# Kernel optimization log

Measured on AMD Instinct MI355X. Metric: run time of the kernel, lower is better.

The kernel has to match this reference:

```python
import math
import jax, jax.numpy as jnp
import numpy as np

NHEAD = 4
EPS = 1e-5


def make_pe(max_len, d):
    pos = np.arange(max_len, dtype=np.float32)[:, None]
    div = np.exp(np.arange(0, d, 2, dtype=np.float32) * (-math.log(10000.0) / d))
    pe = np.zeros((max_len, d), np.float32)
    pe[:, 0::2] = np.sin(pos * div)
    pe[:, 1::2] = np.cos(pos * div)
    return jnp.asarray(pe)


def layer_norm(x, g, b):
    m = jnp.mean(x, axis=-1, keepdims=True)
    v = jnp.mean((x - m) ** 2, axis=-1, keepdims=True)
    return (x - m) / jnp.sqrt(v + EPS) * g + b


def mha(q, k, v, wq, bq, wk, bk, wv, bv, wo, bo, kmask=None):
    # q: [b, Lq, d], k/v: [b, Lk, d]
    b_, lq, d = q.shape
    lk = k.shape[1]
    hd = d // NHEAD
    qh = (q @ wq + bq).reshape(b_, lq, NHEAD, hd)
    kh = (k @ wk + bk).reshape(b_, lk, NHEAD, hd)
    vh = (v @ wv + bv).reshape(b_, lk, NHEAD, hd)
    s = jnp.einsum('bqhd,bkhd->bhqk', qh, kh) / jnp.sqrt(jnp.float32(hd))
    if kmask is not None:
        s = jnp.where(kmask[None, None, None, :], s, jnp.float32(-1e9))
    a = jax.nn.softmax(s, axis=-1)
    o = jnp.einsum('bhqk,bkhd->bqhd', a, vh).reshape(b_, lq, d)
    return o @ wo + bo


def _forward(src, in_w, in_b, dec_start,
             e_wq, e_bq, e_wk, e_bk, e_wv, e_bv, e_wo, e_bo,
             e_ln1_g, e_ln1_b, e_w1, e_b1, e_w2, e_b2, e_ln2_g, e_ln2_b,
             d_swq, d_sbq, d_swk, d_sbk, d_swv, d_sbv, d_swo, d_sbo,
             d_ln1_g, d_ln1_b,
             d_cwq, d_cbq, d_cwk, d_cbk, d_cwv, d_cbv, d_cwo, d_cbo,
             d_ln2_g, d_ln2_b,
             d_w1, d_b1, d_w2, d_b2, d_ln3_g, d_ln3_b,
             out_w, out_b, tgt_len):
    B, S = src.shape
    d = in_w.shape[1]
    T = tgt_len
    pe = make_pe(max(S, T) + 10, d)

    # ---- encoder (1 post-norm layer, relu FFN, dropout off) ----
    x = (src[..., None] @ in_w + in_b) * jnp.sqrt(jnp.float32(d))  # [B,S,d]
    x = x + pe[None, :S]
    x = layer_norm(x + mha(x, x, x, e_wq, e_bq, e_wk, e_bk, e_wv, e_bv, e_wo, e_bo), e_ln1_g, e_ln1_b)
    mem = layer_norm(x + (jax.nn.relu(x @ e_w1 + e_b1) @ e_w2 + e_b2), e_ln2_g, e_ln2_b)

    buf0 = jnp.zeros((B, T + 1, d), src.dtype).at[:, 0].set(dec_start[0, 0])
    pe_dec = pe[None, :T + 1]
    kidx = jnp.arange(T + 1)

    def step(buf, t):
        di = buf + pe_dec
        kmask = kidx <= t  # full (non-causal) attention over the t+1 valid tokens
        h = layer_norm(di + mha(di, di, di, d_swq, d_sbq, d_swk, d_sbk,
                                d_swv, d_sbv, d_swo, d_sbo, kmask=kmask),
                       d_ln1_g, d_ln1_b)
        h = layer_norm(h + mha(h, mem, mem, d_cwq, d_cbq, d_cwk, d_cbk,
                               d_cwv, d_cbv, d_cwo, d_cbo),
                       d_ln2_g, d_ln2_b)
        h = layer_norm(h + (jax.nn.relu(h @ d_w1 + d_b1) @ d_w2 + d_b2),
                       d_ln3_g, d_ln3_b)
        last = h[:, t]                       # [B,d] output at the newest position
        buf = buf.at[:, t + 1].set(last)     # feed back as next decoder token
        y = (last @ out_w + out_b)[:, 0]     # [B]
        return buf, y

    _, outs = jax.lax.scan(step, buf0, jnp.arange(T))  # outs: [T,B]
    return outs.T  # [B,T]


def setup_inputs():
    B, S, T, d, ff = 128, 512, 64, 48, 128
    ks = iter(jax.random.split(jax.random.key(0), 64))

    def w(shape, s=0.08):
        return jax.random.normal(next(ks), shape, jnp.float32) * s

    ones = lambda: jnp.ones((d,), jnp.float32)
    zeros = lambda: jnp.zeros((d,), jnp.float32)
    return dict(
        src=jax.random.normal(next(ks), (B, S), jnp.float32),
        in_w=w((1, d)), in_b=w((d,)),
        dec_start=w((1, 1, d), 1.0),
        e_wq=w((d, d)), e_bq=w((d,)), e_wk=w((d, d)), e_bk=w((d,)),
        e_wv=w((d, d)), e_bv=w((d,)), e_wo=w((d, d)), e_bo=w((d,)),
        e_ln1_g=ones(), e_ln1_b=zeros(),
        e_w1=w((d, ff)), e_b1=w((ff,)), e_w2=w((ff, d)), e_b2=w((d,)),
        e_ln2_g=ones(), e_ln2_b=zeros(),
        d_swq=w((d, d)), d_sbq=w((d,)), d_swk=w((d, d)), d_sbk=w((d,)),
        d_swv=w((d, d)), d_sbv=w((d,)), d_swo=w((d, d)), d_sbo=w((d,)),
        d_ln1_g=ones(), d_ln1_b=zeros(),
        d_cwq=w((d, d)), d_cbq=w((d,)), d_cwk=w((d, d)), d_cbk=w((d,)),
        d_cwv=w((d, d)), d_cbv=w((d,)), d_cwo=w((d, d)), d_cbo=w((d,)),
        d_ln2_g=ones(), d_ln2_b=zeros(),
        d_w1=w((d, ff)), d_b1=w((ff,)), d_w2=w((ff, d)), d_b2=w((d,)),
        d_ln3_g=ones(), d_ln3_b=zeros(),
        out_w=w((d, 1)), out_b=w((1,)),
        tgt_len=T,
    )


def reference(src, in_w, in_b, dec_start,
              e_wq, e_bq, e_wk, e_bk, e_wv, e_bv, e_wo, e_bo,
              e_ln1_g, e_ln1_b, e_w1, e_b1, e_w2, e_b2, e_ln2_g, e_ln2_b,
              d_swq, d_sbq, d_swk, d_sbk, d_swv, d_sbv, d_swo, d_sbo,
              d_ln1_g, d_ln1_b,
              d_cwq, d_cbq, d_cwk, d_cbk, d_cwv, d_cbv, d_cwo, d_cbo,
              d_ln2_g, d_ln2_b,
              d_w1, d_b1, d_w2, d_b2, d_ln3_g, d_ln3_b,
              out_w, out_b, tgt_len):
    return _forward(src, in_w, in_b, dec_start,
                    e_wq, e_bq, e_wk, e_bk, e_wv, e_bv, e_wo, e_bo,
                    e_ln1_g, e_ln1_b, e_w1, e_b1, e_w2, e_b2, e_ln2_g, e_ln2_b,
                    d_swq, d_sbq, d_swk, d_sbk, d_swv, d_sbv, d_swo, d_sbo,
                    d_ln1_g, d_ln1_b,
                    d_cwq, d_cbq, d_cwk, d_cbk, d_cwv, d_cbv, d_cwo, d_cbo,
                    d_ln2_g, d_ln2_b,
                    d_w1, d_b1, d_w2, d_b2, d_ln3_g, d_ln3_b,
                    out_w, out_b, tgt_len)
```

## Files before the change

kernel.cpp:

```cpp
#include <hip/hip_runtime.h>
#include <hip/hip_bf16.h>
#include <hip/hip_fp16.h>


constexpr int kB  = 128;
constexpr int kS  = 512;
constexpr int kT  = 64;
constexpr int kD  = 48;
constexpr int kFF = 128;
constexpr int kNH = 4;
constexpr int kHD = 12;

__device__ __forceinline__ void wsync(){
  __builtin_amdgcn_wave_barrier();
  asm volatile("" ::: "memory");
}

template<int CTRL,int RM,int BM,bool BC>
__device__ __forceinline__ float dppmov(float x, float old){
  return __builtin_bit_cast(float, __builtin_amdgcn_update_dpp(
      __builtin_bit_cast(int, old), __builtin_bit_cast(int, x), CTRL, RM, BM, BC));
}
__device__ __forceinline__ float wsum(float x){
  x += dppmov<0x111,0xf,0xf,true>(x, 0.f);
  x += dppmov<0x112,0xf,0xf,true>(x, 0.f);
  x += dppmov<0x114,0xf,0xf,true>(x, 0.f);
  x += dppmov<0x118,0xf,0xf,true>(x, 0.f);
  x += dppmov<0x142,0xa,0xf,true>(x, 0.f);
  x += dppmov<0x143,0xc,0xf,true>(x, 0.f);
  return __builtin_bit_cast(float, __builtin_amdgcn_readlane(__builtin_bit_cast(int, x), 63));
}
__device__ __forceinline__ float rowsum16(float x){
  x += dppmov<0x111,0xf,0xf,true>(x, 0.f);
  x += dppmov<0x112,0xf,0xf,true>(x, 0.f);
  x += dppmov<0x114,0xf,0xf,true>(x, 0.f);
  x += dppmov<0x118,0xf,0xf,true>(x, 0.f);
  return x;
}

__device__ __forceinline__ float pe_val(int p, int j){
  int i = j >> 1;
  float f = expf(-0.19188209108283716f * (float)(2*i));
  float a = (float)p * f;
  return (j & 1) ? cosf(a) : sinf(a);
}
__device__ __forceinline__ float pe_fast(int p, int j){
  int i = j >> 1;
  float f = __expf(-0.19188209108283716f * (float)(2*i));
  float a = (float)p * f;
  return (j & 1) ? __cosf(a) : __sinf(a);
}

typedef _Float16 h2v __attribute__((ext_vector_type(2)));
union H2U { __half2 h; h2v v; };
__device__ __forceinline__ float fdot2(__half2 a, __half2 b, float c){
#if __has_builtin(__builtin_amdgcn_fdot2)
  H2U ua, ub; ua.h=a; ub.h=b;
  return __builtin_amdgcn_fdot2(ua.v, ub.v, c, false);
#else
  float2 fa=__half22float2(a), fb=__half22float2(b);
  return fmaf(fa.y, fb.y, fmaf(fa.x, fb.x, c));
#endif
}

__device__ __forceinline__ float dot48d(const __half2* x, const __half* w){
  const __half2* w2=(const __half2*)w;
  float a0=0.f,a1=0.f,a2=0.f,a3=0.f;
  #pragma unroll
  for(int c=0;c<6;c++){
    a0=fdot2(x[4*c+0],w2[4*c+0],a0);
    a1=fdot2(x[4*c+1],w2[4*c+1],a1);
    a2=fdot2(x[4*c+2],w2[4*c+2],a2);
    a3=fdot2(x[4*c+3],w2[4*c+3],a3);
  }
  return (a0+a1)+(a2+a3);
}
__device__ __forceinline__ float dot128d(const __half2* x, const __half* w){
  const __half2* w2=(const __half2*)w;
  float a0=0.f,a1=0.f,a2=0.f,a3=0.f,a4=0.f,a5=0.f,a6=0.f,a7=0.f;
  #pragma unroll
  for(int c=0;c<8;c++){
    a0=fdot2(x[8*c+0],w2[8*c+0],a0);
    a1=fdot2(x[8*c+1],w2[8*c+1],a1);
    a2=fdot2(x[8*c+2],w2[8*c+2],a2);
    a3=fdot2(x[8*c+3],w2[8*c+3],a3);
    a4=fdot2(x[8*c+4],w2[8*c+4],a4);
    a5=fdot2(x[8*c+5],w2[8*c+5],a5);
    a6=fdot2(x[8*c+6],w2[8*c+6],a6);
    a7=fdot2(x[8*c+7],w2[8*c+7],a7);
  }
  return ((a0+a1)+(a2+a3))+((a4+a5)+(a6+a7));
}

__global__ void __launch_bounds__(256) k_qkv(const float* __restrict__ src,
    const float* __restrict__ in_w, const float* __restrict__ in_b,
    float* __restrict__ X0,
    const float* __restrict__ wq, const float* __restrict__ bq,
    const float* __restrict__ wk, const float* __restrict__ bk,
    const float* __restrict__ wv, const float* __restrict__ bv,
    __half* __restrict__ Q, __half* __restrict__ K, __half* __restrict__ V){
  __shared__ __align__(16) __half W[3*2688];
  __shared__ __align__(16) float bias[3*kD];
  __shared__ __align__(16) __half2 xt2[32*24];
  int tid = threadIdx.x;
  for (int i=tid;i<3*2304;i+=256){ int m=i/2304, e=i%2304, k=e/48, j=e%48;
    const float* w = (m==0)?wq:((m==1)?wk:wv);
    W[m*2688 + j*56 + k] = __float2half(w[e]); }
  for (int i=tid;i<3*kD;i+=256){ int m=i/kD,e=i%kD;
    const float* w=(m==0)?bq:((m==1)?bk:bv); bias[i]=w[e]; }
  long row0 = (long)blockIdx.x*32;
  const float sc = 6.928203230275509f;
  for (int i=tid;i<768;i+=256){
    int r=i/24, c=i%24;
    long gr=row0+r; int s=(int)(gr&511);
    float sv=src[gr];
    float va=(sv*in_w[2*c  ]+in_b[2*c  ])*sc + pe_fast(s,2*c  );
    float vb=(sv*in_w[2*c+1]+in_b[2*c+1])*sc + pe_fast(s,2*c+1);
    ((float2*)X0)[row0*24 + i]=make_float2(va,vb);
    xt2[i]=__floats2half2_rn(va,vb);
  }
  __syncthreads();
  int r = tid>>3, c0 = tid&7;
  __half2 xr[24];
  #pragma unroll
  for(int u=0;u<24;u++) xr[u]=xt2[r*24+u];
  for (int c=c0; c<3*kD; c+=8){
    int m=c/kD, j=c%kD;
    float acc = bias[m*kD+j] + dot48d(xr, W + m*2688 + j*56);
    __half* o = (m==0)?Q:((m==1)?K:V);
    o[(row0+r)*kD+j]=__float2half(acc);
  }
}

__global__ void __launch_bounds__(256) k_attn(const __half* Q, const __half* __restrict__ K,
                       const __half* __restrict__ V, __half* O){
  int b = blockIdx.x / kNH, h = blockIdx.x % kNH;
  __shared__ __align__(16) __half2 Ks2[kS*6];
  __shared__ __align__(16) float   Vs[kS*kHD];
  int tid = threadIdx.x;
  long base = ((long)b*kS)*kD + h*kHD;
  for (int i=tid;i<kS*6;i+=256){ int r=i/6, c=i%6;
    Ks2[i]=*(const __half2*)&K[base+(long)r*kD+2*c]; }
  for (int i=tid;i<kS*kHD;i+=256){ int r=i/kHD, d=i%kHD;
    Vs[i]=__half2float(V[base+(long)r*kD+d]); }
  const float rs = 0.28867513459481287f;
  int q0 = tid, q1 = tid+256;
  __half2 qa2[6], qb2[6];
  {
    const __half2* qp0=(const __half2*)(Q+base+(long)q0*kD);
    const __half2* qp1=(const __half2*)(Q+base+(long)q1*kD);
    #pragma unroll
    for(int c=0;c<6;c++){ qa2[c]=qp0[c]; qb2[c]=qp1[c]; }
  }
  __syncthreads();
  float2 acc0[6], acc1[6];
  #pragma unroll
  for(int j=0;j<6;j++){ acc0[j]=make_float2(0.f,0.f); acc1[j]=make_float2(0.f,0.f); }
  float l0=0.f, l1=0.f;
  for(int k=0;k<kS;k++){
    const __half2* kp=Ks2+k*6;
    float sA0=0.f,sA1=0.f,sB0=0.f,sB1=0.f;
    #pragma unroll
    for(int c=0;c<3;c++){
      sA0=fdot2(qa2[2*c],kp[2*c],sA0); sA1=fdot2(qa2[2*c+1],kp[2*c+1],sA1);
      sB0=fdot2(qb2[2*c],kp[2*c],sB0); sB1=fdot2(qb2[2*c+1],kp[2*c+1],sB1);
    }
    float p0=__expf((sA0+sA1)*rs), p1=__expf((sB0+sB1)*rs);
    l0+=p0; l1+=p1;
    const float2* vp=(const float2*)(Vs+k*kHD);
    #pragma unroll
    for(int j=0;j<6;j++){
      float2 v=vp[j];
      acc0[j].x=fmaf(p0,v.x,acc0[j].x); acc0[j].y=fmaf(p0,v.y,acc0[j].y);
      acc1[j].x=fmaf(p1,v.x,acc1[j].x); acc1[j].y=fmaf(p1,v.y,acc1[j].y);
    }
  }
  float i0=1.f/l0, i1=1.f/l1;
  #pragma unroll
  for(int j=0;j<6;j++){
    O[base+(long)q0*kD+2*j  ]=__float2half(acc0[j].x*i0);
    O[base+(long)q0*kD+2*j+1]=__float2half(acc0[j].y*i0);
    O[base+(long)q1*kD+2*j  ]=__float2half(acc1[j].x*i1);
    O[base+(long)q1*kD+2*j+1]=__float2half(acc1[j].y*i1);
  }
}

__global__ void __launch_bounds__(256) k_oproj_ln(const float* __restrict__ Xres, const __half* __restrict__ O,
      const float* __restrict__ wo, const float* __restrict__ bo,
      const float* __restrict__ g, const float* __restrict__ bb,
      __half* __restrict__ Xout){
  __shared__ __align__(16) __half W[kD*56];
  __shared__ float bsh[kD], gs[kD], bs2[kD];
  __shared__ __align__(16) float res[32*kD];
  __shared__ __align__(16) __half2 ot2[32*24];
  __shared__ float mrow[32], rstd[32];
  int tid=threadIdx.x;
  for(int i=tid;i<kD*kD;i+=256){ int k=i/48, j=i%48; W[j*56+k]=__float2half(wo[i]); }
  if(tid<kD){ bsh[tid]=bo[tid]; gs[tid]=g[tid]; bs2[tid]=bb[tid]; }
  long row0=(long)blockIdx.x*32;
  const __half2* Op=(const __half2*)(O+row0*kD);
  for(int i=tid;i<768;i+=256) ot2[i]=Op[i];
  __syncthreads();
  int r=tid>>3, c0=tid&7;
  __half2 orow[24];
  #pragma unroll
  for(int u=0;u<24;u++) orow[u]=ot2[r*24+u];
  for(int j=c0;j<kD;j+=8){
    float acc=bsh[j]+dot48d(orow, W+j*56);
    res[r*kD+j]=Xres[row0*kD + r*kD + j]+acc;
  }
  __syncthreads();
  if(tid<32){
    float s=0.f, s2=0.f;
    for(int j=0;j<kD;j++){ float v=res[tid*kD+j]; s+=v; s2+=v*v; }
    float m=s*(1.f/kD);
    mrow[tid]=m; rstd[tid]=rsqrtf(s2*(1.f/kD)-m*m+1e-5f);
  }
  __syncthreads();
  for(int i=tid;i<32*kD;i+=256){int r2=i/kD,j=i%kD;
    Xout[row0*kD+i]=__float2half((res[i]-mrow[r2])*rstd[r2]*gs[j]+bs2[j]); }
}

__global__ void __launch_bounds__(256) k_ffn_ln(const __half* __restrict__ Xin,
   const float* __restrict__ w1, const float* __restrict__ b1,
   const float* __restrict__ w2, const float* __restrict__ b2,
   const float* __restrict__ g, const float* __restrict__ bb,
   float* __restrict__ Xout){
  __shared__ __align__(16) __half W1[kFF*56];
  __shared__ __align__(16) __half W2[kD*136];
  __shared__ float b1s[kFF], b2s[kD], gs[kD], bs2[kD];
  __shared__ __align__(16) __half xt[16*kD];
  __shared__ __align__(16) __half h1h[16*kFF];
  __shared__ __align__(16) float res[16*kD];
  __shared__ float mrow[16], rstd[16];
  int tid=threadIdx.x;
  for(int i=tid;i<kD*kFF;i+=256){ int k=i/128, c=i%128; W1[c*56+k]=__float2half(w1[i]); }
  for(int i=tid;i<kFF*kD;i+=256){ int u=i/48, j=i%48; W2[j*136+u]=__float2half(w2[i]); }
  if(tid<kFF) b1s[tid]=b1[tid];
  if(tid<kD){ b2s[tid]=b2[tid]; gs[tid]=g[tid]; bs2[tid]=bb[tid]; }
  long row0=(long)blockIdx.x*16;
  const __half2* Xp=(const __half2*)(Xin+row0*kD);
  for(int i=tid;i<384;i+=256) ((__half2*)xt)[i]=Xp[i];
  __syncthreads();
  int r=tid>>4, c0=tid&15;
  {
    __half2 xr[24];
    const __half2* xp=(const __half2*)(xt + r*kD);
    #pragma unroll
    for(int u=0;u<24;u++) xr[u]=xp[u];
    for(int c=c0;c<kFF;c+=16){
      float acc=b1s[c]+dot48d(xr, W1+c*56);
      h1h[r*kFF+c]=__float2half(fmaxf(acc,0.f));
    }
  }
  __syncthreads();
  {
    const __half2* hp=(const __half2*)(h1h + r*kFF);
    for(int j=c0;j<kD;j+=16){
      float acc=b2s[j]+dot128d(hp, W2+j*136);
      res[r*kD+j]=__half2float(xt[r*kD+j])+acc;
    }
  }
  __syncthreads();
  if(tid<16){
    float s=0.f, s2=0.f;
    for(int j=0;j<kD;j++){ float v=res[tid*kD+j]; s+=v; s2+=v*v; }
    float m=s*(1.f/kD);
    mrow[tid]=m; rstd[tid]=rsqrtf(s2*(1.f/kD)-m*m+1e-5f);
  }
  __syncthreads();
  for(int i=tid;i<16*kD;i+=256){int r2=i/kD,j=i%kD;
    Xout[row0*kD+i]=(res[i]-mrow[r2])*rstd[r2]*gs[j]+bs2[j]; }
}

__global__ void __launch_bounds__(256) k_ckv(const float* __restrict__ M,
    const float* __restrict__ wk, const float* __restrict__ bk,
    const float* __restrict__ wv, const float* __restrict__ bv,
    __half* __restrict__ Kc, __half* __restrict__ Vc){
  __shared__ __align__(16) __half W[2*2688];
  __shared__ float bias[2*kD];
  __shared__ __align__(16) __half2 xt2[32*24];
  int tid=threadIdx.x;
  for(int i=tid;i<2*2304;i+=256){ int m=i/2304, e=i%2304, k=e/48, j=e%48;
    W[m*2688 + j*56 + k] = __float2half((m?wv:wk)[e]); }
  for(int i=tid;i<2*kD;i+=256){ int m=i/kD,e=i%kD; bias[i]=(m?bv:bk)[e]; }
  long row0=(long)blockIdx.x*32;
  const float2* Mp=(const float2*)(M+row0*kD);
  for(int i=tid;i<768;i+=256){ float2 v=Mp[i]; xt2[i]=__floats2half2_rn(v.x,v.y); }
  __syncthreads();
  int r=tid>>3, c0=tid&7;
  __half2 xr[24];
  #pragma unroll
  for(int u=0;u<24;u++) xr[u]=xt2[r*24+u];
  long gr=row0+r; long bb2=gr>>9; long s=gr&511;
  for(int c=c0;c<2*kD;c+=8){
    int m=c/kD, j=c%kD;
    float acc=bias[m*kD+j]+dot48d(xr, W+m*2688+j*56);
    if(m==0) Kc[(bb2*kS+s)*kD + j]=__float2half(acc);
    else     Vc[(bb2*kD+j)*kS + s]=__float2half(acc);
  }
}

__global__ void k_prep(const float* __restrict__ swq,const float* __restrict__ swk,
                       const float* __restrict__ swv,const float* __restrict__ swo,
                       const float* __restrict__ cwq,const float* __restrict__ cwo,
                       const float* __restrict__ w1,const float* __restrict__ w2,
                       __half* __restrict__ Wh){
  int idx=blockIdx.x*256+threadIdx.x;
  if(idx>=26112) return;
  if(idx<13824){
    int m=idx/2304, e=idx%2304, j=e/48, k=e%48;
    const float* w = (m==0)?swq:((m==1)?swk:((m==2)?swv:((m==3)?swo:((m==4)?cwq:cwo))));
    Wh[m*2688 + j*56 + k] = __float2half(w[k*48+j]);
  } else if(idx<19968){
    int e=idx-13824, c=e/48, k=e%48;
    Wh[16128 + c*56 + k] = __float2half(w1[k*128+c]);
  } else {
    int e=idx-19968, j=e/128, u=e%128;
    Wh[23296 + j*136 + u] = __float2half(w2[u*48+j]);
  }
}

struct DecP {
  const float *dec_start, *sbq, *sbk, *sbv, *sbo, *ln1g, *ln1b,
              *cbq, *cbo, *ln2g, *ln2b, *fb1, *fb2, *ln3g, *ln3b, *ow, *ob;
};

__global__ void __launch_bounds__(256,1) k_dec(const __half* __restrict__ KT,
    const __half* __restrict__ VT, const __half* __restrict__ Wg, DecP P,
    float* __restrict__ out){
  __shared__ __align__(16) __half Wl[29824];
  __shared__ __align__(16) float peT[kT*kD];
  __shared__ __align__(16) __half KhH[kNH*kT*kHD];
  __shared__ __align__(16) float  Vh[kNH*kT*kHD];
  __shared__ __align__(16) __half qSH[kNH*kHD];
  __shared__ __align__(16) __half xvH[kD], soH[kD], h1H[kD], cqH[kD], covH[kD], h2H[kD];
  __shared__ __align__(16) __half f1H[kFF];
  int tid=threadIdx.x, b=blockIdx.x, wave=tid>>6, lane=tid&63;
  const float rs=0.28867513459481287f;

  for(int i=tid;i<29824/8;i+=256) ((float4*)Wl)[i]=((const float4*)Wg)[i];
  for(int i=tid;i<kT*kD;i+=256){ int tt=i/kD, j=i%kD; peT[i]=pe_val(tt,j); }

  float c_sbq=0,c_sbk=0,c_sbv=0, c_bo=0,c_cbq=0,c_cbo=0,c_fb2=0;
  float g1=0,bb1=0,g2=0,bb2=0,g3=0,bb3=0,c_ow=0, c_fb1a=0,c_fb1b=0, c_ds=0;
  if(wave==0){
    if(lane<kD){
      c_ds=P.dec_start[lane];
      c_sbq=P.sbq[lane]; c_sbk=P.sbk[lane]; c_sbv=P.sbv[lane];
      c_bo=P.sbo[lane]; c_cbq=P.cbq[lane]; c_cbo=P.cbo[lane]; c_fb2=P.fb2[lane];
      g1=P.ln1g[lane]; bb1=P.ln1b[lane];
      g2=P.ln2g[lane]; bb2=P.ln2b[lane];
      g3=P.ln3g[lane]; bb3=P.ln3b[lane];
      c_ow=P.ow[lane];
    }
    c_fb1a=P.fb1[lane]; c_fb1b=P.fb1[lane+64];
  }
  float c_ob=P.ob[0];

  __half2 Kr2[4][2][6], Vr2[4][kHD];
  {
    const __half* Kb = KT + (long)b*kS*kD;
    const __half2* Vb = (const __half2*)VT + (long)b*kD*(kS/2);
    #pragma unroll
    for(int i=0;i<4;i++){
      int sp = lane + 64*i;
      #pragma unroll
      for(int e=0;e<2;e++){
        const __half2* kp=(const __half2*)(Kb + (long)(2*sp+e)*kD + wave*kHD);
        #pragma unroll
        for(int c=0;c<6;c++) Kr2[i][e][c]=kp[c];
      }
      #pragma unroll
      for(int u=0;u<kHD;u++) Vr2[i][u]=Vb[(wave*kHD+u)*(kS/2)+sp];
    }
  }
  __syncthreads();

  float xv=0;
  if(wave==0 && lane<kD){ xv=c_ds+peT[lane]; xvH[lane]=__float2half(xv); }
  __syncthreads();

  float h1=0, h2=0, yacc=0;
  for(int t=0;t<kT;t++){
    if(wave==0){
      if(lane<kD){
        __half2 xr[24];
        const __half2* xp=(const __half2*)xvH;
        #pragma unroll
        for(int u=0;u<24;u++) xr[u]=xp[u];
        float qv=c_sbq+dot48d(xr, Wl + 0*2688 + lane*56);
        float kv=c_sbk+dot48d(xr, Wl + 1*2688 + lane*56);
        float vv=c_sbv+dot48d(xr, Wl + 2*2688 + lane*56);
        int hh=lane/kHD, dd=lane%kHD;
        qSH[lane]=__float2half(qv);
        KhH[(hh*kT+t)*kHD+dd]=__float2half(kv);
        Vh[(hh*kT+t)*kHD+dd]=vv;
      }
      wsync();
      {
        int hh=lane>>4, g=lane&15;
        __half2 q2[6];
        const __half2* qp=(const __half2*)qSH + hh*6;
        #pragma unroll
        for(int c=0;c<6;c++) q2[c]=qp[c];
        float l=0.f, acc[kHD];
        #pragma unroll
        for(int u=0;u<kHD;u++) acc[u]=0.f;
        #pragma unroll
        for(int kk=0;kk<4;kk++){
          int key=g+16*kk;
          if(key<=t){
            const __half2* kp=(const __half2*)KhH + (hh*kT+key)*6;
            float a0=0.f,a1=0.f;
            a0=fdot2(q2[0],kp[0],a0); a1=fdot2(q2[1],kp[1],a1);
            a0=fdot2(q2[2],kp[2],a0); a1=fdot2(q2[3],kp[3],a1);
            a0=fdot2(q2[4],kp[4],a0); a1=fdot2(q2[5],kp[5],a1);
            float p=__expf((a0+a1)*rs);
            l+=p;
            const float4* vp=(const float4*)(Vh+(hh*kT+key)*kHD);
            float4 v0=vp[0], v1=vp[1], v2=vp[2];
            float vr[kHD]={v0.x,v0.y,v0.z,v0.w,v1.x,v1.y,v1.z,v1.w,v2.x,v2.y,v2.z,v2.w};
            #pragma unroll
            for(int u=0;u<kHD;u++) acc[u]+=p*vr[u];
          }
        }
        l=rowsum16(l);
        #pragma unroll
        for(int u=0;u<kHD;u++) acc[u]=rowsum16(acc[u]);
        if(g==15){
          float inv=1.f/l;
          #pragma unroll
          for(int u=0;u<6;u++)
            ((__half2*)soH)[hh*6+u]=__floats2half2_rn(acc[2*u]*inv, acc[2*u+1]*inv);
        }
      }
      wsync();
      {
        float rr=0.f;
        if(lane<kD)
          rr=xv+c_bo+dot48d((const __half2*)soH, Wl+8064+lane*56);
        float s1=wsum(rr), s2=wsum(rr*rr);
        float mean=s1*(1.f/48.f);
        float rstd=rsqrtf(s2*(1.f/48.f)-mean*mean+1e-5f);
        h1=0;
        if(lane<kD){ h1=(rr-mean)*rstd*g1+bb1; h1H[lane]=__float2half(h1); }
      }
      wsync();
      if(lane<kD)
        cqH[lane]=__float2half(c_cbq+dot48d((const __half2*)h1H, Wl+10752+lane*56));
    }
    __syncthreads();
    {
      __half2 q2[6];
      #pragma unroll
      for(int c=0;c<6;c++) q2[c]=((const __half2*)cqH)[wave*6+c];
      float s[8];
      #pragma unroll
      for(int i=0;i<4;i++){
        #pragma unroll
        for(int e=0;e<2;e++){
          float a0=0.f,a1=0.f;
          const __half2* kp=Kr2[i][e];
          a0=fdot2(q2[0],kp[0],a0); a1=fdot2(q2[1],kp[1],a1);
          a0=fdot2(q2[2],kp[2],a0); a1=fdot2(q2[3],kp[3],a1);
          a0=fdot2(q2[4],kp[4],a0); a1=fdot2(q2[5],kp[5],a1);
          s[2*i+e]=(a0+a1)*rs;
        }
      }
      float p32[8], l=0.f;
      #pragma unroll
      for(int j=0;j<8;j++){ p32[j]=__expf(s[j]); l+=p32[j]; }
      l=wsum(l);
      float inv=1.f/l;
      __half2 ph[4];
      #pragma unroll
      for(int i=0;i<4;i++) ph[i]=__floats2half2_rn(p32[2*i]*inv, p32[2*i+1]*inv);
      float acc[kHD];
      #pragma unroll
      for(int u=0;u<kHD;u++) acc[u]=0.f;
      #pragma unroll
      for(int i=0;i<4;i++){
        #pragma unroll
        for(int u=0;u<kHD;u++) acc[u]=fdot2(ph[i],Vr2[i][u],acc[u]);
      }
      #pragma unroll
      for(int u=0;u<kHD;u++) acc[u]=wsum(acc[u]);
      if(lane==0){
        #pragma unroll
        for(int u=0;u<6;u++)
          ((__half2*)covH)[wave*6+u]=__floats2half2_rn(acc[2*u], acc[2*u+1]);
      }
    }
    __syncthreads();
    if(wave==0){
      {
        float rr=0.f;
        if(lane<kD)
          rr=h1+c_cbo+dot48d((const __half2*)covH, Wl+13440+lane*56);
        float s1=wsum(rr), s2=wsum(rr*rr);
        float mean=s1*(1.f/48.f);
        float rstd=rsqrtf(s2*(1.f/48.f)-mean*mean+1e-5f);
        h2=0;
        if(lane<kD){ h2=(rr-mean)*rstd*g2+bb2; h2H[lane]=__float2half(h2); }
      }
      wsync();
      {
        float a=c_fb1a+dot48d((const __half2*)h2H, Wl+16128+lane*56);
        float bcol=c_fb1b+dot48d((const __half2*)h2H, Wl+16128+(lane+64)*56);
        f1H[lane]=__float2half(fmaxf(a,0.f));
        f1H[lane+64]=__float2half(fmaxf(bcol,0.f));
      }
      wsync();
      {
        float rr=0.f;
        if(lane<kD)
          rr=h2+c_fb2+dot128d((const __half2*)f1H, Wl+23296+lane*136);
        float s1=wsum(rr), s2=wsum(rr*rr);
        float mean=s1*(1.f/48.f);
        float rstd=rsqrtf(s2*(1.f/48.f)-mean*mean+1e-5f);
        float cv=0.f;
        if(lane<kD) cv=(rr-mean)*rstd*g3+bb3;
        if(lane<kD && t+1<kT){ xv=cv+peT[(t+1)*kD+lane]; xvH[lane]=__float2half(xv); }
        wsync();
        float y=wsum(cv*c_ow);
        if(lane==t) yacc=y;
      }
    }
  }
  if(wave==0) out[(long)b*kT+lane]=yacc+c_ob;
}

extern "C" void kernel_launch(void* const* d_in, const int* in_sizes, int n_in,
                              void* d_out, int out_size, void* d_ws, size_t ws_size,
                              hipStream_t stream){
  float* ws = (float*)d_ws;
  __half* Wh = (__half*)ws;
  const size_t NB = (size_t)kB*kS*kD;
  float*  A  = ws + 16384;
  __half* H1 = (__half*)(A + NB);
  __half* H2 = H1 + NB;
  __half* H3 = H2 + NB;

  k_qkv  <<<(kB*kS)/32,256,0,stream>>>((const float*)d_in[0],(const float*)d_in[1],(const float*)d_in[2],A,
                                       (const float*)d_in[4],(const float*)d_in[5],(const float*)d_in[6],
                                       (const float*)d_in[7],(const float*)d_in[8],(const float*)d_in[9],H1,H2,H3);
  k_attn <<<kB*kNH,256,0,stream>>>(H1,H2,H3,H1);
  k_oproj_ln<<<(kB*kS)/32,256,0,stream>>>(A,H1,(const float*)d_in[10],(const float*)d_in[11],
                                          (const float*)d_in[12],(const float*)d_in[13],H2);
  k_ffn_ln  <<<(kB*kS)/16,256,0,stream>>>(H2,(const float*)d_in[14],(const float*)d_in[15],(const float*)d_in[16],
                                          (const float*)d_in[17],(const float*)d_in[18],(const float*)d_in[19],A);
  k_ckv     <<<(kB*kS)/32,256,0,stream>>>(A,(const float*)d_in[32],(const float*)d_in[33],
                                          (const float*)d_in[34],(const float*)d_in[35],H1,H3);
  k_prep    <<<(26112+255)/256,256,0,stream>>>((const float*)d_in[20],(const float*)d_in[22],(const float*)d_in[24],
                                               (const float*)d_in[26],(const float*)d_in[30],(const float*)d_in[36],
                                               (const float*)d_in[40],(const float*)d_in[42],Wh);
  DecP P;
  P.dec_start=(const float*)d_in[3];
  P.sbq=(const float*)d_in[21]; P.sbk=(const float*)d_in[23]; P.sbv=(const float*)d_in[25]; P.sbo=(const float*)d_in[27];
  P.ln1g=(const float*)d_in[28]; P.ln1b=(const float*)d_in[29];
  P.cbq=(const float*)d_in[31]; P.cbo=(const float*)d_in[37];
  P.ln2g=(const float*)d_in[38]; P.ln2b=(const float*)d_in[39];
  P.fb1=(const float*)d_in[41]; P.fb2=(const float*)d_in[43];
  P.ln3g=(const float*)d_in[44]; P.ln3b=(const float*)d_in[45];
  P.ow=(const float*)d_in[46]; P.ob=(const float*)d_in[47];
  k_dec<<<kB,256,0,stream>>>(H1,H3,Wh,P,(float*)d_out);
}
```

Before: 576.7 us.

## Fuse encoder out-proj, FFN, layernorms and cross K/V projection into one kernel

Merges the output-projection+LN, FFN+LN and cross-attention K/V projection kernels into a single k_post kernel that works on 16-row tiles and keeps intermediates in shared memory. This removes two global round-trips of the [B,S,d] activations and two launches. In exchange each block loads more weights, uses more shared memory and runs at a smaller row tile. The decoder also distributes the cross-attention output projection across all four waves, writing per-head partial sums to shared memory instead of having one wave do the full dot product.

Measured after the change: 607.8 us. +5.4%, slower.

```diff
diff --git a/kernel.cpp b/kernel.cpp
--- a/kernel.cpp
+++ b/kernel.cpp
@@ -185,80 +185,51 @@
   }
 }
 
-__global__ void __launch_bounds__(256) k_oproj_ln(const float* __restrict__ Xres, const __half* __restrict__ O,
-      const float* __restrict__ wo, const float* __restrict__ bo,
-      const float* __restrict__ g, const float* __restrict__ bb,
-      __half* __restrict__ Xout){
-  __shared__ __align__(16) __half W[kD*56];
-  __shared__ float bsh[kD], gs[kD], bs2[kD];
-  __shared__ __align__(16) float res[32*kD];
-  __shared__ __align__(16) __half2 ot2[32*24];
-  __shared__ float mrow[32], rstd[32];
-  int tid=threadIdx.x;
-  for(int i=tid;i<kD*kD;i+=256){ int k=i/48, j=i%48; W[j*56+k]=__float2half(wo[i]); }
-  if(tid<kD){ bsh[tid]=bo[tid]; gs[tid]=g[tid]; bs2[tid]=bb[tid]; }
-  long row0=(long)blockIdx.x*32;
-  const __half2* Op=(const __half2*)(O+row0*kD);
-  for(int i=tid;i<768;i+=256) ot2[i]=Op[i];
-  __syncthreads();
-  int r=tid>>3, c0=tid&7;
-  __half2 orow[24];
-  #pragma unroll
-  for(int u=0;u<24;u++) orow[u]=ot2[r*24+u];
-  for(int j=c0;j<kD;j+=8){
-    float acc=bsh[j]+dot48d(orow, W+j*56);
-    res[r*kD+j]=Xres[row0*kD + r*kD + j]+acc;
-  }
-  __syncthreads();
-  if(tid<32){
-    float s=0.f, s2=0.f;
-    for(int j=0;j<kD;j++){ float v=res[tid*kD+j]; s+=v; s2+=v*v; }
-    float m=s*(1.f/kD);
-    mrow[tid]=m; rstd[tid]=rsqrtf(s2*(1.f/kD)-m*m+1e-5f);
-  }
-  __syncthreads();
-  for(int i=tid;i<32*kD;i+=256){int r2=i/kD,j=i%kD;
-    Xout[row0*kD+i]=__float2half((res[i]-mrow[r2])*rstd[r2]*gs[j]+bs2[j]); }
-}
-
-__global__ void __launch_bounds__(256) k_ffn_ln(const __half* __restrict__ Xin,
-   const float* __restrict__ w1, const float* __restrict__ b1,
-   const float* __restrict__ w2, const float* __restrict__ b2,
-   const float* __restrict__ g, const float* __restrict__ bb,
-   float* __restrict__ Xout){
-  __shared__ __align__(16) __half W1[kFF*56];
-  __shared__ __align__(16) __half W2[kD*136];
-  __shared__ float b1s[kFF], b2s[kD], gs[kD], bs2[kD];
+__global__ void __launch_bounds__(256) k_post(
+    const float* __restrict__ Xres, const __half* __restrict__ O,
+    const float* __restrict__ wo, const float* __restrict__ bo,
+    const float* __restrict__ g1, const float* __restrict__ b1ln,
+    const float* __restrict__ w1, const float* __restrict__ b1,
+    const float* __restrict__ w2, const float* __restrict__ b2,
+    const float* __restrict__ g2, const float* __restrict__ b2ln,
+    const float* __restrict__ wk, const float* __restrict__ bk,
+    const float* __restrict__ wv, const float* __restrict__ bv,
+    __half* __restrict__ Kc, __half* __restrict__ Vc){
+  __shared__ __align__(16) __half Wo[2688];
+  __shared__ __align__(16) __half W1[7168];
+  __shared__ __align__(16) __half W2[6528];
+  __shared__ __align__(16) __half Wk[2688], Wv[2688];
+  __shared__ float bos[kD], g1s[kD], b1lns[kD], b1s[kFF], b2s[kD],
+                   g2s[kD], b2lns[kD], bks[kD], bvs[kD];
+  __shared__ __align__(16) __half2 ot2[16*24];
+  __shared__ __align__(16) float res[16*kD];
   __shared__ __align__(16) __half xt[16*kD];
   __shared__ __align__(16) __half h1h[16*kFF];
-  __shared__ __align__(16) float res[16*kD];
+  __shared__ __align__(16) float res2[16*kD];
+  __shared__ __align__(16) __half memh[16*kD];
   __shared__ float mrow[16], rstd[16];
   int tid=threadIdx.x;
+  for(int i=tid;i<2304;i+=256){ int k=i/48, j=i%48; Wo[j*56+k]=__float2half(wo[i]); }
   for(int i=tid;i<kD*kFF;i+=256){ int k=i/128, c=i%128; W1[c*56+k]=__float2half(w1[i]); }
   for(int i=tid;i<kFF*kD;i+=256){ int u=i/48, j=i%48; W2[j*136+u]=__float2half(w2[i]); }
+  for(int i=tid;i<2304;i+=256){ int k=i/48, j=i%48;
+    Wk[j*56+k]=__float2half(wk[i]); Wv[j*56+k]=__float2half(wv[i]); }
+  if(tid<kD){ bos[tid]=bo[tid]; g1s[tid]=g1[tid]; b1lns[tid]=b1ln[tid];
+    b2s[tid]=b2[tid]; g2s[tid]=g2[tid]; b2lns[tid]=b2ln[tid];
+    bks[tid]=bk[tid]; bvs[tid]=bv[tid]; }
   if(tid<kFF) b1s[tid]=b1[tid];
-  if(tid<kD){ b2s[tid]=b2[tid]; gs[tid]=g[tid]; bs2[tid]=bb[tid]; }
   long row0=(long)blockIdx.x*16;
-  const __half2* Xp=(const __half2*)(Xin+row0*kD);
-  for(int i=tid;i<384;i+=256) ((__half2*)xt)[i]=Xp[i];
+  const __half2* Op=(const __half2*)(O+row0*kD);
+  for(int i=tid;i<384;i+=256) ot2[i]=Op[i];
   __syncthreads();
   int r=tid>>4, c0=tid&15;
   {
-    __half2 xr[24];
-    const __half2* xp=(const __half2*)(xt + r*kD);
-    #pragma unroll
-    for(int u=0;u<24;u++) xr[u]=xp[u];
-    for(int c=c0;c<kFF;c+=16){
-      float acc=b1s[c]+dot48d(xr, W1+c*56);
-      h1h[r*kFF+c]=__float2half(fmaxf(acc,0.f));
-    }
-  }
-  __syncthreads();
-  {
-    const __half2* hp=(const __half2*)(h1h + r*kFF);
+    __half2 orow[24];
+    #pragma unroll
+    for(int u=0;u<24;u++) orow[u]=ot2[r*24+u];
     for(int j=c0;j<kD;j+=16){
-      float acc=b2s[j]+dot128d(hp, W2+j*136);
-      res[r*kD+j]=__half2float(xt[r*kD+j])+acc;
+      float acc=bos[j]+dot48d(orow, Wo+j*56);
+      res[r*kD+j]=Xres[row0*kD + r*kD + j]+acc;
     }
   }
   __syncthreads();
@@ -270,34 +241,49 @@
   }
   __syncthreads();
   for(int i=tid;i<16*kD;i+=256){int r2=i/kD,j=i%kD;
-    Xout[row0*kD+i]=(res[i]-mrow[r2])*rstd[r2]*gs[j]+bs2[j]; }
-}
-
-__global__ void __launch_bounds__(256) k_ckv(const float* __restrict__ M,
-    const float* __restrict__ wk, const float* __restrict__ bk,
-    const float* __restrict__ wv, const float* __restrict__ bv,
-    __half* __restrict__ Kc, __half* __restrict__ Vc){
-  __shared__ __align__(16) __half W[2*2688];
-  __shared__ float bias[2*kD];
-  __shared__ __align__(16) __half2 xt2[32*24];
-  int tid=threadIdx.x;
-  for(int i=tid;i<2*2304;i+=256){ int m=i/2304, e=i%2304, k=e/48, j=e%48;
-    W[m*2688 + j*56 + k] = __float2half((m?wv:wk)[e]); }
-  for(int i=tid;i<2*kD;i+=256){ int m=i/kD,e=i%kD; bias[i]=(m?bv:bk)[e]; }
-  long row0=(long)blockIdx.x*32;
-  const float2* Mp=(const float2*)(M+row0*kD);
-  for(int i=tid;i<768;i+=256){ float2 v=Mp[i]; xt2[i]=__floats2half2_rn(v.x,v.y); }
-  __syncthreads();
-  int r=tid>>3, c0=tid&7;
-  __half2 xr[24];
-  #pragma unroll
-  for(int u=0;u<24;u++) xr[u]=xt2[r*24+u];
-  long gr=row0+r; long bb2=gr>>9; long s=gr&511;
-  for(int c=c0;c<2*kD;c+=8){
-    int m=c/kD, j=c%kD;
-    float acc=bias[m*kD+j]+dot48d(xr, W+m*2688+j*56);
-    if(m==0) Kc[(bb2*kS+s)*kD + j]=__float2half(acc);
-    else     Vc[(bb2*kD+j)*kS + s]=__float2half(acc);
+    xt[i]=__float2half((res[i]-mrow[r2])*rstd[r2]*g1s[j]+b1lns[j]); }
+  __syncthreads();
+  {
+    __half2 xr[24];
+    const __half2* xp=(const __half2*)(xt + r*kD);
+    #pragma unroll
+    for(int u=0;u<24;u++) xr[u]=xp[u];
+    for(int c=c0;c<kFF;c+=16){
+      float acc=b1s[c]+dot48d(xr, W1+c*56);
+      h1h[r*kFF+c]=__float2half(fmaxf(acc,0.f));
+    }
+  }
+  __syncthreads();
+  {
+    const __half2* hp=(const __half2*)(h1h + r*kFF);
+    for(int j=c0;j<kD;j+=16){
+      float acc=b2s[j]+dot128d(hp, W2+j*136);
+      res2[r*kD+j]=__half2float(xt[r*kD+j])+acc;
+    }
+  }
+  __syncthreads();
+  if(tid<16){
+    float s=0.f, s2=0.f;
+    for(int j=0;j<kD;j++){ float v=res2[tid*kD+j]; s+=v; s2+=v*v; }
+    float m=s*(1.f/kD);
+    mrow[tid]=m; rstd[tid]=rsqrtf(s2*(1.f/kD)-m*m+1e-5f);
+  }
+  __syncthreads();
+  for(int i=tid;i<16*kD;i+=256){int r2=i/kD,j=i%kD;
+    memh[i]=__float2half((res2[i]-mrow[r2])*rstd[r2]*g2s[j]+b2lns[j]); }
+  __syncthreads();
+  {
+    __half2 mr[24];
+    const __half2* mp=(const __half2*)(memh + r*kD);
+    #pragma unroll
+    for(int u=0;u<24;u++) mr[u]=mp[u];
+    long gr=row0+r; long bb2=gr>>9; long s=gr&511;
+    for(int c=c0;c<2*kD;c+=16){
+      int m=c/kD, j=c%kD;
+      float acc=(m?bvs:bks)[j]+dot48d(mr, (m?Wv:Wk)+j*56);
+      if(m==0) Kc[(bb2*kS+s)*kD + j]=__float2half(acc);
+      else     Vc[(bb2*kD+j)*kS + s]=__float2half(acc);
+    }
   }
 }
 
@@ -334,7 +320,8 @@
   __shared__ __align__(16) __half KhH[kNH*kT*kHD];
   __shared__ __align__(16) float  Vh[kNH*kT*kHD];
   __shared__ __align__(16) __half qSH[kNH*kHD];
-  __shared__ __align__(16) __half xvH[kD], soH[kD], h1H[kD], cqH[kD], covH[kD], h2H[kD];
+  __shared__ __align__(16) float poS[kNH][kD];
+  __shared__ __align__(16) __half xvH[kD], soH[kD], h1H[kD], cqH[kD], h2H[kD];
   __shared__ __align__(16) __half f1H[kFF];
   int tid=threadIdx.x, b=blockIdx.x, wave=tid>>6, lane=tid&63;
   const float rs=0.28867513459481287f;
@@ -486,10 +473,16 @@
       }
       #pragma unroll
       for(int u=0;u<kHD;u++) acc[u]=wsum(acc[u]);
-      if(lane==0){
-        #pragma unroll
-        for(int u=0;u<6;u++)
-          ((__half2*)covH)[wave*6+u]=__floats2half2_rn(acc[2*u], acc[2*u+1]);
+      if(lane<kD){
+        __half2 ah[6];
+        #pragma unroll
+        for(int u=0;u<6;u++) ah[u]=__floats2half2_rn(acc[2*u],acc[2*u+1]);
+        const __half2* wp=(const __half2*)(Wl+13440+lane*56+wave*kHD);
+        float p0=0.f,p1=0.f;
+        p0=fdot2(ah[0],wp[0],p0); p1=fdot2(ah[1],wp[1],p1);
+        p0=fdot2(ah[2],wp[2],p0); p1=fdot2(ah[3],wp[3],p1);
+        p0=fdot2(ah[4],wp[4],p0); p1=fdot2(ah[5],wp[5],p1);
+        poS[wave][lane]=p0+p1;
       }
     }
     __syncthreads();
@@ -497,7 +490,7 @@
       {
         float rr=0.f;
         if(lane<kD)
-          rr=h1+c_cbo+dot48d((const __half2*)covH, Wl+13440+lane*56);
+          rr=h1+c_cbo+((poS[0][lane]+poS[1][lane])+(poS[2][lane]+poS[3][lane]));
         float s1=wsum(rr), s2=wsum(rr*rr);
         float mean=s1*(1.f/48.f);
         float rstd=rsqrtf(s2*(1.f/48.f)-mean*mean+1e-5f);
@@ -546,12 +539,14 @@
                                        (const float*)d_in[4],(const float*)d_in[5],(const float*)d_in[6],
                                        (const float*)d_in[7],(const float*)d_in[8],(const float*)d_in[9],H1,H2,H3);
   k_attn <<<kB*kNH,256,0,stream>>>(H1,H2,H3,H1);
-  k_oproj_ln<<<(kB*kS)/32,256,0,stream>>>(A,H1,(const float*)d_in[10],(const float*)d_in[11],
-                                          (const float*)d_in[12],(const float*)d_in[13],H2);
-  k_ffn_ln  <<<(kB*kS)/16,256,0,stream>>>(H2,(const float*)d_in[14],(const float*)d_in[15],(const float*)d_in[16],
-                                          (const float*)d_in[17],(const float*)d_in[18],(const float*)d_in[19],A);
-  k_ckv     <<<(kB*kS)/32,256,0,stream>>>(A,(const float*)d_in[32],(const float*)d_in[33],
-                                          (const float*)d_in[34],(const float*)d_in[35],H1,H3);
+  k_post <<<(kB*kS)/16,256,0,stream>>>(A,H1,
+                                       (const float*)d_in[10],(const float*)d_in[11],
+                                       (const float*)d_in[12],(const float*)d_in[13],
+                                       (const float*)d_in[14],(const float*)d_in[15],
+                                       (const float*)d_in[16],(const float*)d_in[17],
+                                       (const float*)d_in[18],(const float*)d_in[19],
+                                       (const float*)d_in[32],(const float*)d_in[33],
+                                       (const float*)d_in[34],(const float*)d_in[35],H2,H3);
   k_prep    <<<(26112+255)/256,256,0,stream>>>((const float*)d_in[20],(const float*)d_in[22],(const float*)d_in[24],
                                                (const float*)d_in[26],(const float*)d_in[30],(const float*)d_in[36],
                                                (const float*)d_in[40],(const float*)d_in[42],Wh);
@@ -564,5 +559,5 @@
   P.fb1=(const float*)d_in[41]; P.fb2=(const float*)d_in[43];
   P.ln3g=(const float*)d_in[44]; P.ln3b=(const float*)d_in[45];
   P.ow=(const float*)d_in[46]; P.ob=(const float*)d_in[47];
-  k_dec<<<kB,256,0,stream>>>(H1,H3,Wh,P,(float*)d_out);
-}
+  k_dec<<<kB,256,0,stream>>>(H2,H3,Wh,P,(float*)d_out);
+}
```

## Split encoder attention over key halves and fold cross-attn out-proj per wave

Applied to the files above, without the earlier changes.

Encoder attention now splits each (batch, head) over two key halves, doubling the grid from 512 to 1024 blocks. Each half writes a normalized partial output and its softmax denominator to new workspace buffers, and the out-projection kernel combines them. No max-subtraction is used, so combining by the denominators is exact. Separately, in the decoder each wave multiplies its own head's cross-attention output by its slice of the output weights into shared memory. Wave 0 then only sums four partials, which shortens the serial work per step. The cost is extra global traffic for the partials and a gather-and-combine step in the out-projection load.

Result: no change. 571.3 us (-0.9%).

```diff
diff --git a/kernel.cpp b/kernel.cpp
--- a/kernel.cpp
+++ b/kernel.cpp
@@ -132,17 +132,21 @@
   }
 }
 
-__global__ void __launch_bounds__(256) k_attn(const __half* Q, const __half* __restrict__ K,
-                       const __half* __restrict__ V, __half* O){
-  int b = blockIdx.x / kNH, h = blockIdx.x % kNH;
-  __shared__ __align__(16) __half2 Ks2[kS*6];
-  __shared__ __align__(16) float   Vs[kS*kHD];
+__global__ void __launch_bounds__(256) k_attn(const __half* __restrict__ Q,
+      const __half* __restrict__ K, const __half* __restrict__ V,
+      __half* __restrict__ OP, float* __restrict__ lP){
+  int part = blockIdx.x & 1;
+  int bh = blockIdx.x >> 1;
+  int b = bh / kNH, h = bh % kNH;
+  __shared__ __align__(16) __half2 Ks2[256*6];
+  __shared__ __align__(16) float   Vs[256*kHD];
   int tid = threadIdx.x;
   long base = ((long)b*kS)*kD + h*kHD;
-  for (int i=tid;i<kS*6;i+=256){ int r=i/6, c=i%6;
-    Ks2[i]=*(const __half2*)&K[base+(long)r*kD+2*c]; }
-  for (int i=tid;i<kS*kHD;i+=256){ int r=i/kHD, d=i%kHD;
-    Vs[i]=__half2float(V[base+(long)r*kD+d]); }
+  int k0 = part<<8;
+  for (int i=tid;i<256*6;i+=256){ int r=i/6, c=i%6;
+    Ks2[i]=*(const __half2*)&K[base+(long)(k0+r)*kD+2*c]; }
+  for (int i=tid;i<256*kHD;i+=256){ int r=i/kHD, d=i%kHD;
+    Vs[i]=__half2float(V[base+(long)(k0+r)*kD+d]); }
   const float rs = 0.28867513459481287f;
   int q0 = tid, q1 = tid+256;
   __half2 qa2[6], qb2[6];
@@ -157,7 +161,7 @@
   #pragma unroll
   for(int j=0;j<6;j++){ acc0[j]=make_float2(0.f,0.f); acc1[j]=make_float2(0.f,0.f); }
   float l0=0.f, l1=0.f;
-  for(int k=0;k<kS;k++){
+  for(int k=0;k<256;k++){
     const __half2* kp=Ks2+k*6;
     float sA0=0.f,sA1=0.f,sB0=0.f,sB1=0.f;
     #pragma unroll
@@ -176,16 +180,21 @@
     }
   }
   float i0=1.f/l0, i1=1.f/l1;
+  const long PS=(long)kB*kNH*kS*kHD, LS=(long)kB*kNH*kS;
+  long ob=((long)(b*kNH+h))*kS;
+  __half2* op0=(__half2*)(OP + part*PS + (ob+q0)*kHD);
+  __half2* op1=(__half2*)(OP + part*PS + (ob+q1)*kHD);
   #pragma unroll
   for(int j=0;j<6;j++){
-    O[base+(long)q0*kD+2*j  ]=__float2half(acc0[j].x*i0);
-    O[base+(long)q0*kD+2*j+1]=__float2half(acc0[j].y*i0);
-    O[base+(long)q1*kD+2*j  ]=__float2half(acc1[j].x*i1);
-    O[base+(long)q1*kD+2*j+1]=__float2half(acc1[j].y*i1);
-  }
-}
-
-__global__ void __launch_bounds__(256) k_oproj_ln(const float* __restrict__ Xres, const __half* __restrict__ O,
+    op0[j]=__floats2half2_rn(acc0[j].x*i0, acc0[j].y*i0);
+    op1[j]=__floats2half2_rn(acc1[j].x*i1, acc1[j].y*i1);
+  }
+  lP[part*LS + ob + q0]=l0;
+  lP[part*LS + ob + q1]=l1;
+}
+
+__global__ void __launch_bounds__(256) k_oproj_ln(const float* __restrict__ Xres,
+      const __half* __restrict__ OP, const float* __restrict__ lP,
       const float* __restrict__ wo, const float* __restrict__ bo,
       const float* __restrict__ g, const float* __restrict__ bb,
       __half* __restrict__ Xout){
@@ -198,8 +207,19 @@
   for(int i=tid;i<kD*kD;i+=256){ int k=i/48, j=i%48; W[j*56+k]=__float2half(wo[i]); }
   if(tid<kD){ bsh[tid]=bo[tid]; gs[tid]=g[tid]; bs2[tid]=bb[tid]; }
   long row0=(long)blockIdx.x*32;
-  const __half2* Op=(const __half2*)(O+row0*kD);
-  for(int i=tid;i<768;i+=256) ot2[i]=Op[i];
+  const long PS=(long)kB*kNH*kS*kHD, LS=(long)kB*kNH*kS;
+  for(int i=tid;i<768;i+=256){
+    int r=i/24, c=i%24;
+    long gq=row0+r; long bb2=gq>>9; long s=gq&511;
+    int h=c/6; int d0=(2*c)%12;
+    long li=(bb2*kNH+h)*kS+s;
+    float l0=lP[li], l1=lP[li+LS];
+    float inv=1.f/(l0+l1);
+    long o0=li*(long)kHD+d0;
+    float v0=(l0*__half2float(OP[o0  ]) + l1*__half2float(OP[o0  +PS]))*inv;
+    float v1=(l0*__half2float(OP[o0+1]) + l1*__half2float(OP[o0+1+PS]))*inv;
+    ot2[i]=__floats2half2_rn(v0,v1);
+  }
   __syncthreads();
   int r=tid>>3, c0=tid&7;
   __half2 orow[24];
@@ -334,7 +354,8 @@
   __shared__ __align__(16) __half KhH[kNH*kT*kHD];
   __shared__ __align__(16) float  Vh[kNH*kT*kHD];
   __shared__ __align__(16) __half qSH[kNH*kHD];
-  __shared__ __align__(16) __half xvH[kD], soH[kD], h1H[kD], cqH[kD], covH[kD], h2H[kD];
+  __shared__ __align__(16) float poS[kNH][kD];
+  __shared__ __align__(16) __half xvH[kD], soH[kD], h1H[kD], cqH[kD], h2H[kD];
   __shared__ __align__(16) __half f1H[kFF];
   int tid=threadIdx.x, b=blockIdx.x, wave=tid>>6, lane=tid&63;
   const float rs=0.28867513459481287f;
@@ -486,10 +507,16 @@
       }
       #pragma unroll
       for(int u=0;u<kHD;u++) acc[u]=wsum(acc[u]);
-      if(lane==0){
-        #pragma unroll
-        for(int u=0;u<6;u++)
-          ((__half2*)covH)[wave*6+u]=__floats2half2_rn(acc[2*u], acc[2*u+1]);
+      if(lane<kD){
+        __half2 ah[6];
+        #pragma unroll
+        for(int u=0;u<6;u++) ah[u]=__floats2half2_rn(acc[2*u],acc[2*u+1]);
+        const __half2* wp=(const __half2*)(Wl+13440+lane*56+wave*kHD);
+        float p0=0.f,p1=0.f;
+        p0=fdot2(ah[0],wp[0],p0); p1=fdot2(ah[1],wp[1],p1);
+        p0=fdot2(ah[2],wp[2],p0); p1=fdot2(ah[3],wp[3],p1);
+        p0=fdot2(ah[4],wp[4],p0); p1=fdot2(ah[5],wp[5],p1);
+        poS[wave][lane]=p0+p1;
       }
     }
     __syncthreads();
@@ -497,7 +524,7 @@
       {
         float rr=0.f;
         if(lane<kD)
-          rr=h1+c_cbo+dot48d((const __half2*)covH, Wl+13440+lane*56);
+          rr=h1+c_cbo+((poS[0][lane]+poS[1][lane])+(poS[2][lane]+poS[3][lane]));
         float s1=wsum(rr), s2=wsum(rr*rr);
         float mean=s1*(1.f/48.f);
         float rstd=rsqrtf(s2*(1.f/48.f)-mean*mean+1e-5f);
@@ -537,16 +564,19 @@
   float* ws = (float*)d_ws;
   __half* Wh = (__half*)ws;
   const size_t NB = (size_t)kB*kS*kD;
+  const size_t BHS = (size_t)kB*kNH*kS;
   float*  A  = ws + 16384;
   __half* H1 = (__half*)(A + NB);
   __half* H2 = H1 + NB;
   __half* H3 = H2 + NB;
+  __half* OP = H3 + NB;
+  float*  lP = (float*)(OP + 2*NB);
 
   k_qkv  <<<(kB*kS)/32,256,0,stream>>>((const float*)d_in[0],(const float*)d_in[1],(const float*)d_in[2],A,
                                        (const float*)d_in[4],(const float*)d_in[5],(const float*)d_in[6],
                                        (const float*)d_in[7],(const float*)d_in[8],(const float*)d_in[9],H1,H2,H3);
-  k_attn <<<kB*kNH,256,0,stream>>>(H1,H2,H3,H1);
-  k_oproj_ln<<<(kB*kS)/32,256,0,stream>>>(A,H1,(const float*)d_in[10],(const float*)d_in[11],
+  k_attn <<<kB*kNH*2,256,0,stream>>>(H1,H2,H3,OP,lP);
+  k_oproj_ln<<<(kB*kS)/32,256,0,stream>>>(A,OP,lP,(const float*)d_in[10],(const float*)d_in[11],
                                           (const float*)d_in[12],(const float*)d_in[13],H2);
   k_ffn_ln  <<<(kB*kS)/16,256,0,stream>>>(H2,(const float*)d_in[14],(const float*)d_in[15],(const float*)d_in[16],
                                           (const float*)d_in[17],(const float*)d_in[18],(const float*)d_in[19],A);
```
